# Kernel optimization log

Measured on AMD Instinct MI355X. Metric: run time of the kernel, lower is better.

Reference implementation:

```python
import jax, jax.numpy as jnp
import numpy as np

N_NODES = 50000  # n_diseases + n_drugs
N_EDGES = 800000
DIM = 64
N_HOPS = 3


def setup_inputs() -> dict:
    key = jax.random.key(0)
    k1, k2, k3, k4 = jax.random.split(key, 4)
    embed = jax.random.normal(k1, (N_NODES, DIM), dtype=jnp.float32)
    row = jax.random.randint(k2, (N_EDGES,), 0, N_NODES)
    col = jax.random.randint(k3, (N_EDGES,), 0, N_NODES)
    edge_index = jnp.stack([row, col]).astype(jnp.int64)
    trend = jax.random.uniform(k4, (N_EDGES,), dtype=jnp.float32)
    return {"embed": embed, "edge_index": edge_index, "trend": trend}


def reference(embed, edge_index, trend):
    # GraphConv_CA: repeated gather(row) -> scale by per-edge trend -> scatter_add(col)
    n = embed.shape[0]
    row, col = edge_index[0], edge_index[1]
    t = trend[:, None]  # [E, 1]

    def hop(agg, _):
        out = agg[row] * t                                      # [E, D] gather + scale
        agg = jax.ops.segment_sum(out, col, num_segments=n)     # [N, D] scatter-add
        return agg, agg

    _, hops = jax.lax.scan(hop, embed, None, length=N_HOPS)     # [H, N, D]
    embs = jnp.concatenate([embed[:, None, :], jnp.moveaxis(hops, 0, 1)], axis=1)  # [N, H+1, D]
    return embs
```

## Files before the change

kernel.cpp:

```cpp
#include <hip/hip_runtime.h>
#include <hip/hip_fp16.h>

#define N_NODES 50000
#define N_EDGES 800000
#define DIM 64
#define OUT_STRIDE 256
#define CAP 64

#define NBUCK 196
#define BCAP 4608
#define ACHUNK 4096
#define ABLOCKS ((N_EDGES + ACHUNK - 1) / ACHUNK)
#define EMBED_F4 (N_NODES * 16)

__device__ __forceinline__ void excl_scan256(int* hist, int* scan, int tid) {
    if (tid < 256) scan[tid] = hist[tid];
    __syncthreads();
    #pragma unroll
    for (int off = 1; off < 256; off <<= 1) {
        int v = 0, u = 0;
        if (tid < 256) { v = scan[tid]; u = (tid >= off) ? scan[tid - off] : 0; }
        __syncthreads();
        if (tid < 256) scan[tid] = v + u;
        __syncthreads();
    }
    if (tid < 256) scan[tid] -= hist[tid];
    __syncthreads();
}

__global__ __launch_bounds__(512) void bucket_partition(const int* __restrict__ row,
                                                        const int* __restrict__ col,
                                                        const float* __restrict__ trend,
                                                        int* __restrict__ gcnt,
                                                        int2* __restrict__ barr) {
    __shared__ int hist[256], scan[256], cur[256], gbase[256];
    __shared__ int2 stage[ACHUNK];
    int tid = threadIdx.x;
    int e0 = blockIdx.x * ACHUNK;
    int ne = N_EDGES - e0; if (ne > ACHUNK) ne = ACHUNK;

    if (tid < 256) hist[tid] = 0;
    __syncthreads();
    for (int j = tid; j < ne; j += 512)
        atomicAdd(&hist[(unsigned)col[e0 + j] >> 8], 1);
    __syncthreads();
    excl_scan256(hist, scan, tid);
    if (tid < 256) {
        cur[tid] = scan[tid];
        gbase[tid] = (tid < NBUCK && hist[tid] > 0) ? atomicAdd(&gcnt[tid], hist[tid]) : 0;
    }
    __syncthreads();
    for (int j = tid; j < ne; j += 512) {
        int c  = col[e0 + j];
        int rr = row[e0 + j];
        float tt = trend[e0 + j];
        int bk = (unsigned)c >> 8, cl = c & 255;
        int s = atomicAdd(&cur[bk], 1);
        stage[s] = make_int2(rr | (cl << 16) | (bk << 24), __float_as_int(tt));
    }
    __syncthreads();
    for (int j = tid; j < ne; j += 512) {
        int2 v = stage[j];
        int bk = (unsigned)v.x >> 24;
        int pos = gbase[bk] + (j - scan[bk]);
        if (pos < BCAP) barr[bk * BCAP + pos] = v;
    }
}

__global__ __launch_bounds__(512) void node_sort_prep(const int* __restrict__ gcnt,
                                                      int2* __restrict__ barr,
                                                      int* __restrict__ starts,
                                                      int* __restrict__ cntc,
                                                      const float4* __restrict__ embed4,
                                                      float4* __restrict__ out4,
                                                      uint2* __restrict__ m0) {
    __shared__ int hist[256], scan[256], cur[256];
    __shared__ int2 stage[BCAP];
    int tid = threadIdx.x;
    int bk = blockIdx.x;
    int base = bk * BCAP;
    int nb = gcnt[bk]; if (nb > BCAP) nb = BCAP;

    if (tid < 256) hist[tid] = 0;
    __syncthreads();
    for (int j = tid; j < nb; j += 512)
        atomicAdd(&hist[((unsigned)barr[base + j].x >> 16) & 255], 1);
    __syncthreads();
    excl_scan256(hist, scan, tid);
    if (tid < 256) cur[tid] = scan[tid];
    __syncthreads();
    for (int j = tid; j < nb; j += 512) {
        int2 v = barr[base + j];
        int cl = ((unsigned)v.x >> 16) & 255;
        int s = atomicAdd(&cur[cl], 1);
        stage[s] = v;
    }
    __syncthreads();
    for (int j = tid; j < nb; j += 512) barr[base + j] = stage[j];
    if (tid < 256) {
        int node = (bk << 8) | tid;
        if (node < N_NODES) {
            starts[node] = base + scan[tid];
            int h = hist[tid]; if (h > CAP) h = CAP;
            cntc[node] = h;
        }
    }
    for (int idx = blockIdx.x * 512 + tid; idx < EMBED_F4; idx += NBUCK * 512) {
        float4 v = embed4[idx];
        out4[(idx >> 4) * 64 + (idx & 15)] = v;
        __half2 a = __floats2half2_rn(v.x, v.y);
        __half2 b = __floats2half2_rn(v.z, v.w);
        uint2 u; u.x = *(unsigned int*)&a; u.y = *(unsigned int*)&b;
        m0[idx] = u;
    }
}

__global__ __launch_bounds__(256) void hop_sorted(const int* __restrict__ starts,
                                                  const int* __restrict__ cntc,
                                                  const int2* __restrict__ barr,
                                                  const uint2* __restrict__ msrc,
                                                  float4* __restrict__ dstf,
                                                  uint2* __restrict__ mdst) {
    int node = (int)((blockIdx.x * 256 + threadIdx.x) >> 6);
    int lane = threadIdx.x & 63;
    if (node >= N_NODES) return;
    int n  = cntc[node];
    int st = starts[node];
    int2 p = barr[st + lane];
    int   r = p.x & 0xFFFF;
    float t = __int_as_float(p.y);
    int g = lane >> 4;
    int piece = lane & 15;

    float4 acc = make_float4(0.f, 0.f, 0.f, 0.f);
    for (int i = 0; i < n; i += 16) {
        #pragma unroll
        for (int s = 0; s < 4; ++s) {
            int idx = i + (s << 2) + g;
            int   ri = __shfl(r, idx);
            float ti = __shfl(t, idx);
            bool valid = idx < n;
            ri = valid ? ri : 0;
            ti = valid ? ti : 0.f;
            uint2 u = msrc[(size_t)ri * 16 + piece];
            __half2 h01 = *reinterpret_cast<__half2*>(&u.x);
            __half2 h23 = *reinterpret_cast<__half2*>(&u.y);
            float2 f01 = __half22float2(h01);
            float2 f23 = __half22float2(h23);
            acc.x = fmaf(f01.x, ti, acc.x);
            acc.y = fmaf(f01.y, ti, acc.y);
            acc.z = fmaf(f23.x, ti, acc.z);
            acc.w = fmaf(f23.y, ti, acc.w);
        }
    }
    #pragma unroll
    for (int off = 16; off <= 32; off <<= 1) {
        acc.x += __shfl_xor(acc.x, off);
        acc.y += __shfl_xor(acc.y, off);
        acc.z += __shfl_xor(acc.z, off);
        acc.w += __shfl_xor(acc.w, off);
    }
    if (g == 0) {
        dstf[(size_t)node * 64 + piece] = acc;
        __half2 a = __floats2half2_rn(acc.x, acc.y);
        __half2 b = __floats2half2_rn(acc.z, acc.w);
        uint2 u; u.x = *(unsigned int*)&a; u.y = *(unsigned int*)&b;
        mdst[(size_t)node * 16 + piece] = u;
    }
}


__global__ __launch_bounds__(256) void init_out_full(const float4* __restrict__ embed4,
                                                     float4* __restrict__ out4) {
    int idx = blockIdx.x * 256 + threadIdx.x;
    if (idx >= N_NODES * 64) return;
    int node = idx >> 6;
    int j = idx & 63;
    float4 v = make_float4(0.f, 0.f, 0.f, 0.f);
    if (j < 16) v = embed4[(node << 4) + j];
    out4[idx] = v;
}

__global__ __launch_bounds__(256) void hop_atomic(const int* __restrict__ row,
                                                  const int* __restrict__ col,
                                                  const float* __restrict__ trend,
                                                  const float* __restrict__ agg_in,
                                                  float* __restrict__ agg_out) {
    int e = (int)((blockIdx.x * 256 + threadIdx.x) >> 6);
    int lane = threadIdx.x & 63;
    if (e >= N_EDGES) return;
    float v = agg_in[(size_t)row[e] * OUT_STRIDE + lane] * trend[e];
    atomicAdd(&agg_out[(size_t)col[e] * OUT_STRIDE + lane], v);
}

extern "C" void kernel_launch(void* const* d_in, const int* in_sizes, int n_in,
                              void* d_out, int out_size, void* d_ws, size_t ws_size,
                              hipStream_t stream) {
    const float* embed = (const float*)d_in[0];
    const int*   edge  = (const int*)d_in[1];
    const float* trend = (const float*)d_in[2];
    const int* row = edge;
    const int* col = edge + N_EDGES;
    float* out = (float*)d_out;

    size_t gcnt_b   = 256 * 4;
    size_t starts_b = (size_t)N_NODES * 4;
    size_t cntc_b   = (size_t)N_NODES * 4;
    size_t mirror_b = (size_t)N_NODES * DIM * 2;
    size_t barr_b   = ((size_t)NBUCK * BCAP + 64) * 8;
    size_t need = gcnt_b + starts_b + cntc_b + 2 * mirror_b + barr_b;

    if (ws_size >= need) {
        char* p = (char*)d_ws;
        int*   gcnt   = (int*)p;              p += gcnt_b;
        int*   starts = (int*)p;              p += starts_b;
        int*   cntc   = (int*)p;              p += cntc_b;
        uint2* mA     = (uint2*)p;            p += mirror_b;
        uint2* mB     = (uint2*)p;            p += mirror_b;
        int2*  barr   = (int2*)p;

        hipMemsetAsync(gcnt, 0, gcnt_b, stream);

        hipLaunchKernelGGL(bucket_partition, dim3(ABLOCKS), dim3(512), 0, stream,
                           row, col, trend, gcnt, barr);
        hipLaunchKernelGGL(node_sort_prep, dim3(NBUCK), dim3(512), 0, stream,
                           gcnt, barr, starts, cntc,
                           (const float4*)embed, (float4*)out, mA);

        int hopBlocks = (N_NODES * 64 + 255) / 256;
        uint2* msrc = mA;
        uint2* mdst = mB;
        for (int h = 1; h <= 3; ++h) {
            hipLaunchKernelGGL(hop_sorted, dim3(hopBlocks), dim3(256), 0, stream,
                               starts, cntc, barr, msrc, (float4*)out + h * 16, mdst);
            uint2* tmp = msrc; msrc = mdst; mdst = tmp;
        }
    } else {
        int initBlocks = (N_NODES * 64 + 255) / 256;
        hipLaunchKernelGGL(init_out_full, dim3(initBlocks), dim3(256), 0, stream,
                           (const float4*)embed, (float4*)out);
        int hopBlocksA = (N_EDGES * 64) / 256;
        for (int h = 1; h <= 3; ++h) {
            hipLaunchKernelGGL(hop_atomic, dim3(hopBlocksA), dim3(256), 0, stream,
                               row, col, trend, out + (h - 1) * DIM, out + h * DIM);
        }
    }
}
```

Before: 96.15 us.

## Split feature dimension into two halves so each hop's gather set fits in cache

The fp16 mirror is split into two 32-dim halves of 3.2 MB each, and the three hops run separately per half in six launches. This shrinks the random-gather working set so it stays resident in L2/MALL. Each wave now processes 8 edges per step with 8 lanes per row. Edge arrays and outputs use nontemporal stores/loads to keep them out of cache, and the last hop skips writing the mirror. The cost is twice as many hop launches and rereading the edge list per half.

```diff
diff --git a/kernel.cpp b/kernel.cpp
--- a/kernel.cpp
+++ b/kernel.cpp
@@ -12,6 +12,12 @@
 #define ACHUNK 4096
 #define ABLOCKS ((N_EDGES + ACHUNK - 1) / ACHUNK)
 #define EMBED_F4 (N_NODES * 16)
+
+typedef float f32x4 __attribute__((ext_vector_type(4)));
+
+__device__ __forceinline__ long long pack_ll(int x, int y) {
+    return (long long)(((unsigned long long)(unsigned)y << 32) | (unsigned)x);
+}
 
 __device__ __forceinline__ void excl_scan256(int* hist, int* scan, int tid) {
     if (tid < 256) scan[tid] = hist[tid];
@@ -32,7 +38,7 @@
                                                         const int* __restrict__ col,
                                                         const float* __restrict__ trend,
                                                         int* __restrict__ gcnt,
-                                                        int2* __restrict__ barr) {
+                                                        long long* __restrict__ barr) {
     __shared__ int hist[256], scan[256], cur[256], gbase[256];
     __shared__ int2 stage[ACHUNK];
     int tid = threadIdx.x;
@@ -63,17 +69,19 @@
         int2 v = stage[j];
         int bk = (unsigned)v.x >> 24;
         int pos = gbase[bk] + (j - scan[bk]);
-        if (pos < BCAP) barr[bk * BCAP + pos] = v;
+        if (pos < BCAP)
+            __builtin_nontemporal_store(pack_ll(v.x, v.y), &barr[bk * BCAP + pos]);
     }
 }
 
 __global__ __launch_bounds__(512) void node_sort_prep(const int* __restrict__ gcnt,
-                                                      int2* __restrict__ barr,
+                                                      long long* __restrict__ barr,
                                                       int* __restrict__ starts,
                                                       int* __restrict__ cntc,
                                                       const float4* __restrict__ embed4,
                                                       float4* __restrict__ out4,
-                                                      uint2* __restrict__ m0) {
+                                                      unsigned long long* __restrict__ mh0,
+                                                      unsigned long long* __restrict__ mh1) {
     __shared__ int hist[256], scan[256], cur[256];
     __shared__ int2 stage[BCAP];
     int tid = threadIdx.x;
@@ -83,20 +91,26 @@
 
     if (tid < 256) hist[tid] = 0;
     __syncthreads();
-    for (int j = tid; j < nb; j += 512)
-        atomicAdd(&hist[((unsigned)barr[base + j].x >> 16) & 255], 1);
+    for (int j = tid; j < nb; j += 512) {
+        long long v = barr[base + j];
+        atomicAdd(&hist[((unsigned)(v & 0xFFFFFFFFu) >> 16) & 255], 1);
+    }
     __syncthreads();
     excl_scan256(hist, scan, tid);
     if (tid < 256) cur[tid] = scan[tid];
     __syncthreads();
     for (int j = tid; j < nb; j += 512) {
-        int2 v = barr[base + j];
-        int cl = ((unsigned)v.x >> 16) & 255;
+        long long v = barr[base + j];
+        int x = (int)(v & 0xFFFFFFFFu);
+        int cl = ((unsigned)x >> 16) & 255;
         int s = atomicAdd(&cur[cl], 1);
-        stage[s] = v;
-    }
-    __syncthreads();
-    for (int j = tid; j < nb; j += 512) barr[base + j] = stage[j];
+        stage[s] = make_int2(x, (int)(v >> 32));
+    }
+    __syncthreads();
+    for (int j = tid; j < nb; j += 512) {
+        int2 v = stage[j];
+        __builtin_nontemporal_store(pack_ll(v.x, v.y), &barr[base + j]);
+    }
     if (tid < 256) {
         int node = (bk << 8) | tid;
         if (node < N_NODES) {
@@ -107,46 +121,50 @@
     }
     for (int idx = blockIdx.x * 512 + tid; idx < EMBED_F4; idx += NBUCK * 512) {
         float4 v = embed4[idx];
-        out4[(idx >> 4) * 64 + (idx & 15)] = v;
-        __half2 a = __floats2half2_rn(v.x, v.y);
-        __half2 b = __floats2half2_rn(v.z, v.w);
-        uint2 u; u.x = *(unsigned int*)&a; u.y = *(unsigned int*)&b;
-        m0[idx] = u;
-    }
-}
-
-__global__ __launch_bounds__(256) void hop_sorted(const int* __restrict__ starts,
-                                                  const int* __restrict__ cntc,
-                                                  const int2* __restrict__ barr,
-                                                  const uint2* __restrict__ msrc,
-                                                  float4* __restrict__ dstf,
-                                                  uint2* __restrict__ mdst) {
+        int node = idx >> 4, j = idx & 15;
+        f32x4 a = {v.x, v.y, v.z, v.w};
+        __builtin_nontemporal_store(a, (f32x4*)&out4[node * 64 + j]);
+        __half2 h01 = __floats2half2_rn(v.x, v.y);
+        __half2 h23 = __floats2half2_rn(v.z, v.w);
+        unsigned long long u = ((unsigned long long)*(unsigned int*)&h23 << 32)
+                             | *(unsigned int*)&h01;
+        unsigned long long* m = (j < 8) ? mh0 : mh1;
+        __builtin_nontemporal_store(u, &m[(size_t)(node << 3) + (j & 7)]);
+    }
+}
+
+__global__ __launch_bounds__(256) void hop_half(const int* __restrict__ starts,
+                                                const int* __restrict__ cntc,
+                                                const long long* __restrict__ barr,
+                                                const unsigned long long* __restrict__ msrc,
+                                                float4* __restrict__ dstf,
+                                                unsigned long long* __restrict__ mdst) {
     int node = (int)((blockIdx.x * 256 + threadIdx.x) >> 6);
     int lane = threadIdx.x & 63;
     if (node >= N_NODES) return;
     int n  = cntc[node];
     int st = starts[node];
-    int2 p = barr[st + lane];
-    int   r = p.x & 0xFFFF;
-    float t = __int_as_float(p.y);
-    int g = lane >> 4;
-    int piece = lane & 15;
+    long long pv = 0;
+    if (lane < n) pv = __builtin_nontemporal_load(&barr[st + lane]);
+    int   r = (int)(pv & 0xFFFF);
+    float t = __int_as_float((int)((unsigned long long)pv >> 32));
+    int g = lane >> 3;
+    int piece = lane & 7;
 
     float4 acc = make_float4(0.f, 0.f, 0.f, 0.f);
-    for (int i = 0; i < n; i += 16) {
+    for (int i = 0; i < n; i += 32) {
         #pragma unroll
         for (int s = 0; s < 4; ++s) {
-            int idx = i + (s << 2) + g;
+            int idx = i + (s << 3) + g;
             int   ri = __shfl(r, idx);
             float ti = __shfl(t, idx);
             bool valid = idx < n;
             ri = valid ? ri : 0;
             ti = valid ? ti : 0.f;
-            uint2 u = msrc[(size_t)ri * 16 + piece];
-            __half2 h01 = *reinterpret_cast<__half2*>(&u.x);
-            __half2 h23 = *reinterpret_cast<__half2*>(&u.y);
-            float2 f01 = __half22float2(h01);
-            float2 f23 = __half22float2(h23);
+            unsigned long long u = msrc[(size_t)(ri << 3) + piece];
+            unsigned int lo = (unsigned int)u, hi = (unsigned int)(u >> 32);
+            float2 f01 = __half22float2(*(__half2*)&lo);
+            float2 f23 = __half22float2(*(__half2*)&hi);
             acc.x = fmaf(f01.x, ti, acc.x);
             acc.y = fmaf(f01.y, ti, acc.y);
             acc.z = fmaf(f23.x, ti, acc.z);
@@ -154,18 +172,22 @@
         }
     }
     #pragma unroll
-    for (int off = 16; off <= 32; off <<= 1) {
+    for (int off = 8; off <= 32; off <<= 1) {
         acc.x += __shfl_xor(acc.x, off);
         acc.y += __shfl_xor(acc.y, off);
         acc.z += __shfl_xor(acc.z, off);
         acc.w += __shfl_xor(acc.w, off);
     }
     if (g == 0) {
-        dstf[(size_t)node * 64 + piece] = acc;
-        __half2 a = __floats2half2_rn(acc.x, acc.y);
-        __half2 b = __floats2half2_rn(acc.z, acc.w);
-        uint2 u; u.x = *(unsigned int*)&a; u.y = *(unsigned int*)&b;
-        mdst[(size_t)node * 16 + piece] = u;
+        f32x4 a = {acc.x, acc.y, acc.z, acc.w};
+        __builtin_nontemporal_store(a, (f32x4*)&dstf[(size_t)node * 64 + piece]);
+        if (mdst) {
+            __half2 h01 = __floats2half2_rn(acc.x, acc.y);
+            __half2 h23 = __floats2half2_rn(acc.z, acc.w);
+            unsigned long long u = ((unsigned long long)*(unsigned int*)&h23 << 32)
+                                 | *(unsigned int*)&h01;
+            __builtin_nontemporal_store(u, &mdst[(size_t)(node << 3) + piece]);
+        }
     }
 }
 
@@ -202,22 +224,25 @@
     const int* row = edge;
     const int* col = edge + N_EDGES;
     float* out = (float*)d_out;
+    float4* out4 = (float4*)out;
 
     size_t gcnt_b   = 256 * 4;
     size_t starts_b = (size_t)N_NODES * 4;
     size_t cntc_b   = (size_t)N_NODES * 4;
-    size_t mirror_b = (size_t)N_NODES * DIM * 2;
+    size_t half_b   = (size_t)N_NODES * 8 * 8;
     size_t barr_b   = ((size_t)NBUCK * BCAP + 64) * 8;
-    size_t need = gcnt_b + starts_b + cntc_b + 2 * mirror_b + barr_b;
+    size_t need = gcnt_b + starts_b + cntc_b + 4 * half_b + barr_b;
 
     if (ws_size >= need) {
         char* p = (char*)d_ws;
-        int*   gcnt   = (int*)p;              p += gcnt_b;
-        int*   starts = (int*)p;              p += starts_b;
-        int*   cntc   = (int*)p;              p += cntc_b;
-        uint2* mA     = (uint2*)p;            p += mirror_b;
-        uint2* mB     = (uint2*)p;            p += mirror_b;
-        int2*  barr   = (int2*)p;
+        int* gcnt   = (int*)p;                       p += gcnt_b;
+        int* starts = (int*)p;                       p += starts_b;
+        int* cntc   = (int*)p;                       p += cntc_b;
+        unsigned long long* mA0 = (unsigned long long*)p;  p += half_b;
+        unsigned long long* mA1 = (unsigned long long*)p;  p += half_b;
+        unsigned long long* mB0 = (unsigned long long*)p;  p += half_b;
+        unsigned long long* mB1 = (unsigned long long*)p;  p += half_b;
+        long long* barr = (long long*)p;
 
         hipMemsetAsync(gcnt, 0, gcnt_b, stream);
 
@@ -225,20 +250,27 @@
                            row, col, trend, gcnt, barr);
         hipLaunchKernelGGL(node_sort_prep, dim3(NBUCK), dim3(512), 0, stream,
                            gcnt, barr, starts, cntc,
-                           (const float4*)embed, (float4*)out, mA);
+                           (const float4*)embed, out4, mA0, mA1);
 
         int hopBlocks = (N_NODES * 64 + 255) / 256;
-        uint2* msrc = mA;
-        uint2* mdst = mB;
-        for (int h = 1; h <= 3; ++h) {
-            hipLaunchKernelGGL(hop_sorted, dim3(hopBlocks), dim3(256), 0, stream,
-                               starts, cntc, barr, msrc, (float4*)out + h * 16, mdst);
-            uint2* tmp = msrc; msrc = mdst; mdst = tmp;
-        }
+        hipLaunchKernelGGL(hop_half, dim3(hopBlocks), dim3(256), 0, stream,
+                           starts, cntc, barr, mA0, out4 + 1 * 16 + 0, mB0);
+        hipLaunchKernelGGL(hop_half, dim3(hopBlocks), dim3(256), 0, stream,
+                           starts, cntc, barr, mB0, out4 + 2 * 16 + 0, mA0);
+        hipLaunchKernelGGL(hop_half, dim3(hopBlocks), dim3(256), 0, stream,
+                           starts, cntc, barr, mA0, out4 + 3 * 16 + 0,
+                           (unsigned long long*)nullptr);
+        hipLaunchKernelGGL(hop_half, dim3(hopBlocks), dim3(256), 0, stream,
+                           starts, cntc, barr, mA1, out4 + 1 * 16 + 8, mB1);
+        hipLaunchKernelGGL(hop_half, dim3(hopBlocks), dim3(256), 0, stream,
+                           starts, cntc, barr, mB1, out4 + 2 * 16 + 8, mA1);
+        hipLaunchKernelGGL(hop_half, dim3(hopBlocks), dim3(256), 0, stream,
+                           starts, cntc, barr, mA1, out4 + 3 * 16 + 8,
+                           (unsigned long long*)nullptr);
     } else {
         int initBlocks = (N_NODES * 64 + 255) / 256;
         hipLaunchKernelGGL(init_out_full, dim3(initBlocks), dim3(256), 0, stream,
-                           (const float4*)embed, (float4*)out);
+                           (const float4*)embed, out4);
         int hopBlocksA = (N_EDGES * 64) / 256;
         for (int h = 1; h <= 3; ++h) {
             hipLaunchKernelGGL(hop_atomic, dim3(hopBlocksA), dim3(256), 0, stream,
```

New measurement: 155.4 us. +61.7%, slower.
